# Optimization experiments

Measured on AMD Instinct MI355X. Metric: run time of the kernel, lower is better.

The kernel has to match this reference:

```python
import jax, jax.numpy as jnp
import numpy as np

NEG_SLOPE = 0.2  # PyG GATConv default negative_slope


def gat_conv(x, src, dst, W, a_src, a_dst, b, concat):
    """One PyG-style GATConv (with self-loops already in src/dst).
    x: [N, F_in], W: [F_in, H*C], a_src/a_dst: [H, C], b: [H*C] or [C].
    """
    N = x.shape[0]
    H, C = a_src.shape
    h = (x @ W).reshape(N, H, C)                      # [N,H,C]
    al_s = jnp.einsum('nhc,hc->nh', h, a_src)         # [N,H]
    al_d = jnp.einsum('nhc,hc->nh', h, a_dst)
    e = al_s[src] + al_d[dst]                         # [E,H]
    e = jnp.where(e >= 0, e, NEG_SLOPE * e)           # leaky_relu
    # softmax over edges grouped by destination node
    emax = jax.ops.segment_max(e, dst, num_segments=N)  # [N,H]
    ex = jnp.exp(e - emax[dst])
    denom = jax.ops.segment_sum(ex, dst, num_segments=N)
    alpha = ex / denom[dst]                           # [E,H]
    msg = h[src] * alpha[:, :, None]                  # [E,H,C]
    out = jax.ops.segment_sum(msg, dst, num_segments=N)  # [N,H,C]
    out = out.reshape(N, H * C) if concat else out.mean(axis=1)
    return out + b


def setup_inputs() -> dict:
    key = jax.random.key(0)
    ks = jax.random.split(key, 10)
    N, E = 100000, 1600000
    F_in, Hc, H, F_out = 128, 64, 2, 64
    x = jax.random.normal(ks[0], (N, F_in), dtype=jnp.float32)
    edge_index = jax.random.randint(ks[1], (2, E), 0, N, dtype=jnp.int64)
    s1 = 1.0 / np.sqrt(F_in)
    W1 = jax.random.uniform(ks[2], (F_in, H * Hc), jnp.float32, -s1, s1)
    a_src1 = jax.random.normal(ks[3], (H, Hc), jnp.float32) * 0.1
    a_dst1 = jax.random.normal(ks[4], (H, Hc), jnp.float32) * 0.1
    b1 = jnp.zeros((H * Hc,), jnp.float32)
    s2 = 1.0 / np.sqrt(H * Hc)
    W2 = jax.random.uniform(ks[5], (H * Hc, H * F_out), jnp.float32, -s2, s2)
    a_src2 = jax.random.normal(ks[6], (H, F_out), jnp.float32) * 0.1
    a_dst2 = jax.random.normal(ks[7], (H, F_out), jnp.float32) * 0.1
    b2 = jnp.zeros((F_out,), jnp.float32)
    return {"x": x, "edge_index": edge_index,
            "W1": W1, "a_src1": a_src1, "a_dst1": a_dst1, "b1": b1,
            "W2": W2, "a_src2": a_src2, "a_dst2": a_dst2, "b2": b2}


def reference(x, edge_index, W1, a_src1, a_dst1, b1, W2, a_src2, a_dst2, b2):
    N = x.shape[0]
    loops = jnp.arange(N, dtype=edge_index.dtype)
    src = jnp.concatenate([edge_index[0], loops])  # PyG GATConv adds self-loops
    dst = jnp.concatenate([edge_index[1], loops])
    h = gat_conv(x, src, dst, W1, a_src1, a_dst1, b1, concat=True)
    h = jax.nn.elu(h)
    out = gat_conv(h, src, dst, W2, a_src2, a_dst2, b2, concat=False)
    return out
```

## Files before the change

### kernel.cpp

```cpp
#include <hip/hip_runtime.h>
#include <hip/hip_fp16.h>

#define NEG_SLOPE 0.2f

typedef _Float16 half4v __attribute__((ext_vector_type(4)));
typedef _Float16 half8v __attribute__((ext_vector_type(8)));
typedef float f32x4 __attribute__((ext_vector_type(4)));

__device__ inline unsigned enc_max(float f) {
    unsigned b = __float_as_uint(f);
    return (b & 0x80000000u) ? ~b : (b | 0x80000000u);
}
__device__ inline float dec_max(unsigned k) {
    return (k & 0x80000000u) ? __uint_as_float(k ^ 0x80000000u)
                             : __uint_as_float(~k);
}

__global__ __launch_bounds__(256) void gemm_al_kernel(
    const float* __restrict__ X, const float* __restrict__ W,
    const float* __restrict__ asrc, const float* __restrict__ adst,
    __half* __restrict__ H16, float* __restrict__ AL,
    unsigned* __restrict__ ubp, int N)
{
    __shared__ alignas(16) char smem[49152];

    const int t = threadIdx.x, lane = t & 63, wave = t >> 6;
    const int r0 = blockIdx.x * 64;

#pragma unroll
    for (int i = 0; i < 8; i++) {
        const int f = t + i * 256;
        const int row = f >> 5, k4 = f & 31;
        const int k8 = k4 >> 1, hf = k4 & 1;
        float4 v = make_float4(0.f, 0.f, 0.f, 0.f);
        if (r0 + row < N) v = ((const float4*)X)[(size_t)(r0 + row) * 32 + k4];
        half4v h = { (_Float16)v.x, (_Float16)v.y, (_Float16)v.z, (_Float16)v.w };
        const int slot = row * 16 + (k8 ^ (row & 7));
        *(half4v*)(smem + slot * 16 + hf * 8) = h;
    }
    {
        const int c = t >> 1, kh = t & 1;
        const float* Wc = W + c;
#pragma unroll
        for (int i8 = 0; i8 < 8; i8++) {
            const int k0 = kh * 64 + i8 * 8;
            half8v h;
#pragma unroll
            for (int j = 0; j < 8; j++) h[j] = (_Float16)Wc[(size_t)(k0 + j) * 128];
            const int slot = c * 16 + ((k0 >> 3) ^ (c & 7));
            *(half8v*)(smem + 16384 + slot * 16) = h;
        }
    }
    __syncthreads();

    const int mrow = wave * 16 + (lane & 15);
    const int kg = lane >> 4;
    half4v a[8];
#pragma unroll
    for (int ks = 0; ks < 8; ks++) {
        const int k0 = ks * 16 + kg * 4;
        const int slot = mrow * 16 + ((k0 >> 3) ^ (mrow & 7));
        a[ks] = *(const half4v*)(smem + slot * 16 + (k0 & 7) * 2);
    }
    f32x4 acc[8];
#pragma unroll
    for (int ct = 0; ct < 8; ct++) acc[ct] = (f32x4){0.f, 0.f, 0.f, 0.f};
#pragma unroll
    for (int ct = 0; ct < 8; ct++) {
        const int c = ct * 16 + (lane & 15);
        const char* sbase = smem + 16384 + c * 256;
        const int csw = c & 7;
#pragma unroll
        for (int ks = 0; ks < 8; ks++) {
            const int k0 = ks * 16 + kg * 4;
            const int slot = (k0 >> 3) ^ csw;
            half4v b = *(const half4v*)(sbase + slot * 16 + (k0 & 7) * 2);
            acc[ct] = __builtin_amdgcn_mfma_f32_16x16x16f16(a[ks], b, acc[ct], 0, 0, 0);
        }
    }

    float psh0[4] = {0,0,0,0}, psh1[4] = {0,0,0,0};
    float pdh0[4] = {0,0,0,0}, pdh1[4] = {0,0,0,0};
#pragma unroll
    for (int ct = 0; ct < 8; ct++) {
        const int c = ct * 16 + (lane & 15);
        const float as = asrc[c], ad = adst[c];
#pragma unroll
        for (int r = 0; r < 4; r++) {
            if (ct < 4) { psh0[r] = fmaf(acc[ct][r], as, psh0[r]);
                          pdh0[r] = fmaf(acc[ct][r], ad, pdh0[r]); }
            else        { psh1[r] = fmaf(acc[ct][r], as, psh1[r]);
                          pdh1[r] = fmaf(acc[ct][r], ad, pdh1[r]); }
        }
    }
#pragma unroll
    for (int off = 1; off <= 8; off <<= 1) {
#pragma unroll
        for (int r = 0; r < 4; r++) {
            psh0[r] += __shfl_xor(psh0[r], off, 64);
            psh1[r] += __shfl_xor(psh1[r], off, 64);
            pdh0[r] += __shfl_xor(pdh0[r], off, 64);
            pdh1[r] += __shfl_xor(pdh1[r], off, 64);
        }
    }
    float rmax0 = -__builtin_inff(), rmax1 = -__builtin_inff();
    if ((lane & 15) == 0) {
#pragma unroll
        for (int r = 0; r < 4; r++) {
            const int gr = r0 + wave * 16 + (lane >> 4) * 4 + r;
            if (gr < N) {
                ((float4*)AL)[gr] = make_float4(psh0[r], psh1[r], pdh0[r], pdh1[r]);
                rmax0 = fmaxf(rmax0, psh0[r]);
                rmax1 = fmaxf(rmax1, psh1[r]);
            }
        }
    }
#pragma unroll
    for (int off = 32; off > 0; off >>= 1) {
        rmax0 = fmaxf(rmax0, __shfl_xor(rmax0, off, 64));
        rmax1 = fmaxf(rmax1, __shfl_xor(rmax1, off, 64));
    }

    __syncthreads();
    float* Dst = (float*)smem;
    float* red = (float*)(smem + 33792);
    if (lane == 0) { red[wave * 2] = rmax0; red[wave * 2 + 1] = rmax1; }
#pragma unroll
    for (int ct = 0; ct < 8; ct++) {
        const int col = ct * 16 + (lane & 15);
        float* drow = Dst + wave * 2112 + ((lane >> 4) * 4) * 132 + col;
#pragma unroll
        for (int r = 0; r < 4; r++) drow[r * 132] = acc[ct][r];
    }
    __syncthreads();
    if (t < 2) {
        float m = fmaxf(fmaxf(red[t], red[2 + t]), fmaxf(red[4 + t], red[6 + t]));
        atomicMax(&ubp[t], enc_max(m));
    }
#pragma unroll
    for (int i = 0; i < 4; i++) {
        const int f = t + i * 256;
        const int row = f >> 4, c16 = f & 15;
        if (r0 + row < N) {
            const float* src = Dst + (row >> 4) * 2112 + (row & 15) * 132 + c16 * 8;
            const float4 v0 = *(const float4*)src;
            const float4 v1 = *(const float4*)(src + 4);
            half8v h = { (_Float16)v0.x, (_Float16)v0.y, (_Float16)v0.z, (_Float16)v0.w,
                         (_Float16)v1.x, (_Float16)v1.y, (_Float16)v1.z, (_Float16)v1.w };
            *(half8v*)((_Float16*)H16 + (size_t)(r0 + row) * 128 + c16 * 8) = h;
        }
    }
}

__global__ void count_kernel(const int* __restrict__ edst, int* __restrict__ cnt,
                             int E, int N)
{
    int i = blockIdx.x * 256 + threadIdx.x;
    if (i < E)            atomicAdd(&cnt[edst[i]], 1);
    else if (i < E + N)   atomicAdd(&cnt[i - E], 1);
}

__global__ void scan_local_kernel(const int* __restrict__ in, int* __restrict__ out,
                                  int* __restrict__ bsum, int n)
{
    __shared__ int sm[1024];
    const int t = threadIdx.x;
    const int i = blockIdx.x * 1024 + t;
    int v = (i < n) ? in[i] : 0;
    sm[t] = v;
    __syncthreads();
    for (int off = 1; off < 1024; off <<= 1) {
        int x = (t >= off) ? sm[t - off] : 0;
        __syncthreads();
        sm[t] += x;
        __syncthreads();
    }
    if (i < n) out[i] = sm[t];
    if (t == 1023) bsum[blockIdx.x] = sm[t];
}

__global__ void scan_excl_single_kernel(int* __restrict__ a, int B)
{
    __shared__ int sm[1024];
    const int t = threadIdx.x;
    int v = (t < B) ? a[t] : 0;
    sm[t] = v;
    __syncthreads();
    for (int off = 1; off < 1024; off <<= 1) {
        int x = (t >= off) ? sm[t - off] : 0;
        __syncthreads();
        sm[t] += x;
        __syncthreads();
    }
    if (t < B) a[t] = sm[t] - v;
}

__global__ void finalize_csr_kernel(const int* __restrict__ incl,
                                    const int* __restrict__ cnt,
                                    const int* __restrict__ bexcl,
                                    int* __restrict__ dstptr, int* __restrict__ cursor,
                                    int N, int Etot)
{
    const int i = blockIdx.x * 1024 + threadIdx.x;
    if (i < N) {
        int v = incl[i] + bexcl[i >> 10] - cnt[i];
        dstptr[i] = v;
        cursor[i] = v;
    }
    if (i == N) dstptr[N] = Etot;
}

__global__ void scatter_kernel(const int* __restrict__ esrc, const int* __restrict__ edst,
                               int* __restrict__ cursor, int* __restrict__ ssrc,
                               int E, int N, int sliceN, int bps)
{
    const int slice = blockIdx.x & 7;
    const int dlo = slice * sliceN;
    const int dhi = min(N, dlo + sliceN);
    const int Etot = E + N;
    for (int i = (blockIdx.x >> 3) * 256 + (int)threadIdx.x; i < Etot; i += bps * 256) {
        int s, d;
        if (i < E) { s = esrc[i]; d = edst[i]; }
        else       { s = d = i - E; }
        if (d >= dlo && d < dhi) {
            int pos = atomicAdd(&cursor[d], 1);
            ssrc[pos] = s;
        }
    }
}

__global__ __launch_bounds__(256) void aggregate_kernel(
    const __half* __restrict__ H16, const float* __restrict__ AL,
    const int* __restrict__ dstptr, const int* __restrict__ ssrc,
    const unsigned* __restrict__ ubenc, const float* __restrict__ bias,
    float* __restrict__ out, int N, int mode)
{
    const int wid  = (blockIdx.x * blockDim.x + threadIdx.x) >> 6;
    const int lane = threadIdx.x & 63;
    if (wid * 2 >= N) return;
    const int nl   = lane & 31;
    const int n    = wid * 2 + (lane >> 5);
    const bool act = (n < N);
    const int nn   = act ? n : (N - 1);
    const int beg  = dstptr[nn];
    const int end  = act ? dstptr[nn + 1] : beg;

    const int head = nl >> 4;
    const float ald = AL[(size_t)nn * 4 + 2 + head];
    float ub = dec_max(ubenc[head]) + ald;
    ub = (ub >= 0.f) ? ub : NEG_SLOPE * ub;

    const int nblk = (end - beg + 3) >> 2;
    const int trips = max(nblk, __shfl_xor(nblk, 32, 64));

    float s = 0.f, a0 = 0.f, a1 = 0.f, a2 = 0.f, a3 = 0.f;

    int sA[4];
    float e0[4], e1[4];
    uint2 g0[4], g1[4];

    auto LSRC = [&](int b, int (&sv)[4]) {
#pragma unroll
        for (int k = 0; k < 4; k++) {
            const int idx = beg + 4 * b + k;
            const int v = ssrc[idx];
            sv[k] = (idx < end) ? v : -1;
        }
    };
    auto LHE = [&](const int (&sv)[4], float (&e)[4], uint2 (&g)[4]) {
#pragma unroll
        for (int k = 0; k < 4; k++) {
            const int src = (sv[k] >= 0) ? sv[k] : 0;
            const float a = AL[(size_t)src * 4 + head];
            e[k] = (sv[k] >= 0) ? a : -__builtin_inff();
            g[k] = ((const uint2*)(H16 + (size_t)src * 128))[nl];
        }
    };

    {
        int ta[4], tb[4];
        LSRC(0, ta); LSRC(1, tb); LSRC(2, sA);
        LHE(ta, e0, g0);
        LHE(tb, e1, g1);
    }

    for (int t = 0; t < trips; t++) {
        int sB[4];
        LSRC(t + 3, sB);
        float e2[4]; uint2 g2[4];
        LHE(sA, e2, g2);
#pragma unroll
        for (int k = 0; k < 4; k++) {
            float tt = e0[k] + ald;
            tt = (tt >= 0.f) ? tt : NEG_SLOPE * tt;
            const float p = __expf(tt - ub);
            s += p;
            const __half2* ph = (const __half2*)&g0[k];
            const float2 f01 = __half22float2(ph[0]);
            const float2 f23 = __half22float2(ph[1]);
            a0 = fmaf(p, f01.x, a0);
            a1 = fmaf(p, f01.y, a1);
            a2 = fmaf(p, f23.x, a2);
            a3 = fmaf(p, f23.y, a3);
        }
#pragma unroll
        for (int k = 0; k < 4; k++) {
            e0[k] = e1[k]; g0[k] = g1[k];
            e1[k] = e2[k]; g1[k] = g2[k];
            sA[k] = sB[k];
        }
    }

    if (!act) return;
    const float inv = 1.f / s;
    float o0 = a0 * inv, o1 = a1 * inv, o2 = a2 * inv, o3 = a3 * inv;

    if (mode == 0) {
        const float4 b4 = ((const float4*)bias)[nl];
        o0 += b4.x; o1 += b4.y; o2 += b4.z; o3 += b4.w;
        o0 = (o0 > 0.f) ? o0 : (__expf(o0) - 1.f);
        o1 = (o1 > 0.f) ? o1 : (__expf(o1) - 1.f);
        o2 = (o2 > 0.f) ? o2 : (__expf(o2) - 1.f);
        o3 = (o3 > 0.f) ? o3 : (__expf(o3) - 1.f);
        ((float4*)out)[(size_t)n * 32 + nl] = make_float4(o0, o1, o2, o3);
    } else {
        const float q0 = __shfl_xor(o0, 16, 64);
        const float q1 = __shfl_xor(o1, 16, 64);
        const float q2 = __shfl_xor(o2, 16, 64);
        const float q3 = __shfl_xor(o3, 16, 64);
        if (nl < 16) {
            const float4 b4 = ((const float4*)bias)[nl];
            ((float4*)out)[(size_t)n * 16 + nl] =
                make_float4(0.5f * (o0 + q0) + b4.x, 0.5f * (o1 + q1) + b4.y,
                            0.5f * (o2 + q2) + b4.z, 0.5f * (o3 + q3) + b4.w);
        }
    }
}

extern "C" void kernel_launch(void* const* d_in, const int* in_sizes, int n_in,
                              void* d_out, int out_size, void* d_ws, size_t ws_size,
                              hipStream_t stream)
{
    const float* x   = (const float*)d_in[0];
    const int*   eix = (const int*)d_in[1];
    const float* W1  = (const float*)d_in[2];
    const float* as1 = (const float*)d_in[3];
    const float* ad1 = (const float*)d_in[4];
    const float* b1  = (const float*)d_in[5];
    const float* W2  = (const float*)d_in[6];
    const float* as2 = (const float*)d_in[7];
    const float* ad2 = (const float*)d_in[8];
    const float* b2  = (const float*)d_in[9];
    float* out = (float*)d_out;

    const int N = in_sizes[0] / 128;
    const int E = in_sizes[1] / 2;
    const int Etot = E + N;
    const int* esrc = eix;
    const int* edst = eix + E;

    char* p = (char*)d_ws;
    __half*   h16    = (__half*)p;   p += (size_t)N * 128 * 2;
    float*    y1     = (float*)p;    p += (size_t)N * 128 * 4;
    float*    al     = (float*)p;    p += (size_t)N * 4 * 4;
    int*      cnt    = (int*)p;      p += (size_t)N * 4;
    unsigned* ub     = (unsigned*)p; p += 64;
    int*      incl   = (int*)p;      p += (size_t)N * 4;
    int*      dstptr = (int*)p;      p += (size_t)(N + 1) * 4;
    int*      cursor = (int*)p;      p += (size_t)N * 4;
    int*      bs1    = (int*)p;      p += 1024 * 4;
    int*      ssrc   = (int*)p;      p += (size_t)(Etot + 256) * 4;

    hipMemsetAsync(cnt, 0, (size_t)N * 4 + 64, stream);

    {
        const int eblocks = (Etot + 255) / 256;
        const int B0 = (N + 1023) / 1024;
        count_kernel<<<eblocks, 256, 0, stream>>>(edst, cnt, E, N);
        scan_local_kernel<<<B0, 1024, 0, stream>>>(cnt, incl, bs1, N);
        scan_excl_single_kernel<<<1, 1024, 0, stream>>>(bs1, B0);
        finalize_csr_kernel<<<(N + 1024) / 1024, 1024, 0, stream>>>(
            incl, cnt, bs1, dstptr, cursor, N, Etot);
        const int sliceN = (N + 7) / 8;
        const int bps = 512;
        scatter_kernel<<<bps * 8, 256, 0, stream>>>(esrc, edst, cursor, ssrc,
                                                    E, N, sliceN, bps);
    }

    const int ggrid = (N + 63) / 64;
    const int nwaves = (N + 1) / 2;
    const int ablocks = (nwaves + 3) / 4;

    gemm_al_kernel<<<ggrid, 256, 0, stream>>>(x, W1, as1, ad1, h16, al, ub, N);
    aggregate_kernel<<<ablocks, 256, 0, stream>>>(h16, al, dstptr, ssrc, ub, b1, y1, N, 0);

    gemm_al_kernel<<<ggrid, 256, 0, stream>>>(y1, W2, as2, ad2, h16, al, ub + 2, N);
    aggregate_kernel<<<ablocks, 256, 0, stream>>>(h16, al, dstptr, ssrc, ub + 2, b2, out, N, 1);
}
```

Measured before the change: 377.0 us.

## Map one wavefront per destination node in GAT aggregation with exp2 softmax

The aggregation kernel now gives each destination node a full 64-lane wavefront, with each lane holding two fp16 features, instead of packing two nodes per wave at four features per lane. Each node now loops over its own edge count instead of the larger count of the paired node. The gather pipeline rotates through three register buffers rather than copying them. Per-edge index masking is replaced by a zero-padded tail in the source array plus a zero weight for out-of-range edges. Attention coefficients are pre-scaled by log2(e) in the GEMM so the softmax can use exp2f. The trade-off is twice as many waves with narrower 4-byte gathers per lane, which may increase instruction and scheduling overhead.

```diff
diff --git a/kernel.cpp b/kernel.cpp
--- a/kernel.cpp
+++ b/kernel.cpp
@@ -2,6 +2,7 @@
 #include <hip/hip_fp16.h>
 
 #define NEG_SLOPE 0.2f
+#define LOG2E 1.4426950408889634f
 
 typedef _Float16 half4v __attribute__((ext_vector_type(4)));
 typedef _Float16 half8v __attribute__((ext_vector_type(8)));
@@ -84,7 +85,7 @@
 #pragma unroll
     for (int ct = 0; ct < 8; ct++) {
         const int c = ct * 16 + (lane & 15);
-        const float as = asrc[c], ad = adst[c];
+        const float as = asrc[c] * LOG2E, ad = adst[c] * LOG2E;
 #pragma unroll
         for (int r = 0; r < 4; r++) {
             if (ct < 4) { psh0[r] = fmaf(acc[ct][r], as, psh0[r]);
@@ -229,110 +230,82 @@
     }
 }
 
-__global__ __launch_bounds__(256) void aggregate_kernel(
+__global__ __launch_bounds__(128) void aggregate_kernel(
     const __half* __restrict__ H16, const float* __restrict__ AL,
     const int* __restrict__ dstptr, const int* __restrict__ ssrc,
     const unsigned* __restrict__ ubenc, const float* __restrict__ bias,
     float* __restrict__ out, int N, int mode)
 {
-    const int wid  = (blockIdx.x * blockDim.x + threadIdx.x) >> 6;
+    const int n = (blockIdx.x * blockDim.x + threadIdx.x) >> 6;
     const int lane = threadIdx.x & 63;
-    if (wid * 2 >= N) return;
-    const int nl   = lane & 31;
-    const int n    = wid * 2 + (lane >> 5);
-    const bool act = (n < N);
-    const int nn   = act ? n : (N - 1);
-    const int beg  = dstptr[nn];
-    const int end  = act ? dstptr[nn + 1] : beg;
-
-    const int head = nl >> 4;
-    const float ald = AL[(size_t)nn * 4 + 2 + head];
+    if (n >= N) return;
+
+    const int beg = dstptr[n], end = dstptr[n + 1];
+    const int head = lane >> 5;
+    const float ald = AL[(size_t)n * 4 + 2 + head];
     float ub = dec_max(ubenc[head]) + ald;
-    ub = (ub >= 0.f) ? ub : NEG_SLOPE * ub;
+    ub = fmaxf(ub, NEG_SLOPE * ub);
 
     const int nblk = (end - beg + 3) >> 2;
-    const int trips = max(nblk, __shfl_xor(nblk, 32, 64));
-
-    float s = 0.f, a0 = 0.f, a1 = 0.f, a2 = 0.f, a3 = 0.f;
-
-    int sA[4];
-    float e0[4], e1[4];
-    uint2 g0[4], g1[4];
+
+    float s = 0.f, a0 = 0.f, a1 = 0.f;
+
+    int   sv0[4], sv1[4], sv2[4];
+    float e0[4], e1[4], e2[4];
+    unsigned g0[4], g1[4], g2[4];
 
     auto LSRC = [&](int b, int (&sv)[4]) {
 #pragma unroll
+        for (int k = 0; k < 4; k++) sv[k] = ssrc[beg + 4 * b + k];
+    };
+    auto LHE = [&](const int (&sv)[4], float (&e)[4], unsigned (&g)[4]) {
+#pragma unroll
         for (int k = 0; k < 4; k++) {
-            const int idx = beg + 4 * b + k;
-            const int v = ssrc[idx];
-            sv[k] = (idx < end) ? v : -1;
+            e[k] = AL[(size_t)sv[k] * 4 + head];
+            g[k] = ((const unsigned*)(H16 + (size_t)sv[k] * 128))[lane];
         }
     };
-    auto LHE = [&](const int (&sv)[4], float (&e)[4], uint2 (&g)[4]) {
+    auto COMP = [&](int t, const float (&e)[4], const unsigned (&g)[4]) {
+        const int rem = end - (beg + 4 * t);
 #pragma unroll
         for (int k = 0; k < 4; k++) {
-            const int src = (sv[k] >= 0) ? sv[k] : 0;
-            const float a = AL[(size_t)src * 4 + head];
-            e[k] = (sv[k] >= 0) ? a : -__builtin_inff();
-            g[k] = ((const uint2*)(H16 + (size_t)src * 128))[nl];
+            float tt = e[k] + ald;
+            tt = fmaxf(tt, NEG_SLOPE * tt);
+            float p = exp2f(tt - ub);
+            p = (k < rem) ? p : 0.f;
+            s += p;
+            const float2 f = __half22float2(*(const __half2*)&g[k]);
+            a0 = fmaf(p, f.x, a0);
+            a1 = fmaf(p, f.y, a1);
         }
     };
 
-    {
-        int ta[4], tb[4];
-        LSRC(0, ta); LSRC(1, tb); LSRC(2, sA);
-        LHE(ta, e0, g0);
-        LHE(tb, e1, g1);
-    }
-
-    for (int t = 0; t < trips; t++) {
-        int sB[4];
-        LSRC(t + 3, sB);
-        float e2[4]; uint2 g2[4];
-        LHE(sA, e2, g2);
-#pragma unroll
-        for (int k = 0; k < 4; k++) {
-            float tt = e0[k] + ald;
-            tt = (tt >= 0.f) ? tt : NEG_SLOPE * tt;
-            const float p = __expf(tt - ub);
-            s += p;
-            const __half2* ph = (const __half2*)&g0[k];
-            const float2 f01 = __half22float2(ph[0]);
-            const float2 f23 = __half22float2(ph[1]);
-            a0 = fmaf(p, f01.x, a0);
-            a1 = fmaf(p, f01.y, a1);
-            a2 = fmaf(p, f23.x, a2);
-            a3 = fmaf(p, f23.y, a3);
-        }
-#pragma unroll
-        for (int k = 0; k < 4; k++) {
-            e0[k] = e1[k]; g0[k] = g1[k];
-            e1[k] = e2[k]; g1[k] = g2[k];
-            sA[k] = sB[k];
-        }
-    }
-
-    if (!act) return;
+    LSRC(0, sv0); LSRC(1, sv1); LSRC(2, sv2);
+    LHE(sv0, e0, g0);
+    LHE(sv1, e1, g1);
+
+    for (int t = 0; t < nblk; ) {
+        LHE(sv2, e2, g2); LSRC(t + 3, sv0); COMP(t, e0, g0); if (++t == nblk) break;
+        LHE(sv0, e0, g0); LSRC(t + 3, sv1); COMP(t, e1, g1); if (++t == nblk) break;
+        LHE(sv1, e1, g1); LSRC(t + 3, sv2); COMP(t, e2, g2); if (++t == nblk) break;
+    }
+
     const float inv = 1.f / s;
-    float o0 = a0 * inv, o1 = a1 * inv, o2 = a2 * inv, o3 = a3 * inv;
+    float o0 = a0 * inv, o1 = a1 * inv;
 
     if (mode == 0) {
-        const float4 b4 = ((const float4*)bias)[nl];
-        o0 += b4.x; o1 += b4.y; o2 += b4.z; o3 += b4.w;
+        const float2 b2 = ((const float2*)bias)[lane];
+        o0 += b2.x; o1 += b2.y;
         o0 = (o0 > 0.f) ? o0 : (__expf(o0) - 1.f);
         o1 = (o1 > 0.f) ? o1 : (__expf(o1) - 1.f);
-        o2 = (o2 > 0.f) ? o2 : (__expf(o2) - 1.f);
-        o3 = (o3 > 0.f) ? o3 : (__expf(o3) - 1.f);
-        ((float4*)out)[(size_t)n * 32 + nl] = make_float4(o0, o1, o2, o3);
+        ((float2*)out)[(size_t)n * 64 + lane] = make_float2(o0, o1);
     } else {
-        const float q0 = __shfl_xor(o0, 16, 64);
-        const float q1 = __shfl_xor(o1, 16, 64);
-        const float q2 = __shfl_xor(o2, 16, 64);
-        const float q3 = __shfl_xor(o3, 16, 64);
-        if (nl < 16) {
-            const float4 b4 = ((const float4*)bias)[nl];
-            ((float4*)out)[(size_t)n * 16 + nl] =
-                make_float4(0.5f * (o0 + q0) + b4.x, 0.5f * (o1 + q1) + b4.y,
-                            0.5f * (o2 + q2) + b4.z, 0.5f * (o3 + q3) + b4.w);
+        const float q0 = __shfl_xor(o0, 32, 64);
+        const float q1 = __shfl_xor(o1, 32, 64);
+        if (lane < 32) {
+            const float2 b2 = ((const float2*)bias)[lane];
+            ((float2*)out)[(size_t)n * 32 + lane] =
+                make_float2(0.5f * (o0 + q0) + b2.x, 0.5f * (o1 + q1) + b2.y);
         }
     }
 }
@@ -372,6 +345,7 @@
     int*      ssrc   = (int*)p;      p += (size_t)(Etot + 256) * 4;
 
     hipMemsetAsync(cnt, 0, (size_t)N * 4 + 64, stream);
+    hipMemsetAsync(ssrc + Etot, 0, 256 * 4, stream);
 
     {
         const int eblocks = (Etot + 255) / 256;
@@ -388,12 +362,11 @@
     }
 
     const int ggrid = (N + 63) / 64;
-    const int nwaves = (N + 1) / 2;
-    const int ablocks = (nwaves + 3) / 4;
+    const int ablocks = (N + 1) / 2;
 
     gemm_al_kernel<<<ggrid, 256, 0, stream>>>(x, W1, as1, ad1, h16, al, ub, N);
-    aggregate_kernel<<<ablocks, 256, 0, stream>>>(h16, al, dstptr, ssrc, ub, b1, y1, N, 0);
+    aggregate_kernel<<<ablocks, 128, 0, stream>>>(h16, al, dstptr, ssrc, ub, b1, y1, N, 0);
 
     gemm_al_kernel<<<ggrid, 256, 0, stream>>>(y1, W2, as2, ad2, h16, al, ub + 2, N);
-    aggregate_kernel<<<ablocks, 256, 0, stream>>>(h16, al, dstptr, ssrc, ub + 2, b2, out, N, 1);
-}
+    aggregate_kernel<<<ablocks, 128, 0, stream>>>(h16, al, dstptr, ssrc, ub + 2, b2, out, N, 1);
+}
```

Result: slower. 404.7 us (+7.3%).

## Sort destination nodes by degree for balanced aggregation and simplify gather loop

Applied to the files above, without the earlier changes.

Builds a counting-sort permutation of destination nodes by in-degree during CSR construction, so each wave's two half-wave nodes have similar edge counts and do less divergent idle work. The aggregate loop drops per-edge validity masks on loads by zero-padding the tail of ssrc, and masks only the computed weight. It also rotates three register buffers instead of copying them, and folds log2(e) into the attention coefficients so exp2f replaces __expf. The cost is extra histogram and atomic work in the scan and finalize kernels, plus an indirect order lookup that scatters output writes.

```diff
diff --git a/kernel.cpp b/kernel.cpp
--- a/kernel.cpp
+++ b/kernel.cpp
@@ -2,6 +2,7 @@
 #include <hip/hip_fp16.h>
 
 #define NEG_SLOPE 0.2f
+#define LOG2E 1.4426950408889634f
 
 typedef _Float16 half4v __attribute__((ext_vector_type(4)));
 typedef _Float16 half8v __attribute__((ext_vector_type(8)));
@@ -84,7 +85,7 @@
 #pragma unroll
     for (int ct = 0; ct < 8; ct++) {
         const int c = ct * 16 + (lane & 15);
-        const float as = asrc[c], ad = adst[c];
+        const float as = asrc[c] * LOG2E, ad = adst[c] * LOG2E;
 #pragma unroll
         for (int r = 0; r < 4; r++) {
             if (ct < 4) { psh0[r] = fmaf(acc[ct][r], as, psh0[r]);
@@ -161,14 +162,17 @@
 }
 
 __global__ void scan_local_kernel(const int* __restrict__ in, int* __restrict__ out,
-                                  int* __restrict__ bsum, int n)
+                                  int* __restrict__ bsum, int* __restrict__ hist, int n)
 {
     __shared__ int sm[1024];
+    __shared__ int lh[256];
     const int t = threadIdx.x;
     const int i = blockIdx.x * 1024 + t;
+    if (t < 256) lh[t] = 0;
     int v = (i < n) ? in[i] : 0;
     sm[t] = v;
     __syncthreads();
+    if (i < n) atomicAdd(&lh[min(v, 255)], 1);
     for (int off = 1; off < 1024; off <<= 1) {
         int x = (t >= off) ? sm[t - off] : 0;
         __syncthreads();
@@ -177,9 +181,11 @@
     }
     if (i < n) out[i] = sm[t];
     if (t == 1023) bsum[blockIdx.x] = sm[t];
-}
-
-__global__ void scan_excl_single_kernel(int* __restrict__ a, int B)
+    if (t < 256 && lh[t]) atomicAdd(&hist[t], lh[t]);
+}
+
+__global__ void scan_excl_single_kernel(int* __restrict__ a, int B,
+                                        int* __restrict__ hist)
 {
     __shared__ int sm[1024];
     const int t = threadIdx.x;
@@ -193,21 +199,48 @@
         __syncthreads();
     }
     if (t < B) a[t] = sm[t] - v;
+    __syncthreads();
+    int h = (t < 256) ? hist[t] : 0;
+    sm[t] = h;
+    __syncthreads();
+    for (int off = 1; off < 256; off <<= 1) {
+        int x = (t >= off && t < 256) ? sm[t - off] : 0;
+        __syncthreads();
+        if (t < 256) sm[t] += x;
+        __syncthreads();
+    }
+    if (t < 256) hist[t] = sm[t] - h;
 }
 
 __global__ void finalize_csr_kernel(const int* __restrict__ incl,
                                     const int* __restrict__ cnt,
                                     const int* __restrict__ bexcl,
                                     int* __restrict__ dstptr, int* __restrict__ cursor,
+                                    int* __restrict__ hist, int* __restrict__ order,
                                     int N, int Etot)
 {
-    const int i = blockIdx.x * 1024 + threadIdx.x;
+    __shared__ int lh[256], lbase[256];
+    const int t = threadIdx.x;
+    const int i = blockIdx.x * 1024 + t;
+    if (t < 256) lh[t] = 0;
+    __syncthreads();
+    int bin = 0;
     if (i < N) {
-        int v = incl[i] + bexcl[i >> 10] - cnt[i];
+        const int c = cnt[i];
+        const int v = incl[i] + bexcl[i >> 10] - c;
         dstptr[i] = v;
         cursor[i] = v;
+        bin = min(c, 255);
+        atomicAdd(&lh[bin], 1);
     }
     if (i == N) dstptr[N] = Etot;
+    __syncthreads();
+    if (t < 256) { lbase[t] = lh[t] ? atomicAdd(&hist[t], lh[t]) : 0; lh[t] = 0; }
+    __syncthreads();
+    if (i < N) {
+        const int off = atomicAdd(&lh[bin], 1);
+        order[lbase[bin] + off] = i;
+    }
 }
 
 __global__ void scatter_kernel(const int* __restrict__ esrc, const int* __restrict__ edst,
@@ -232,70 +265,55 @@
 __global__ __launch_bounds__(256) void aggregate_kernel(
     const __half* __restrict__ H16, const float* __restrict__ AL,
     const int* __restrict__ dstptr, const int* __restrict__ ssrc,
-    const unsigned* __restrict__ ubenc, const float* __restrict__ bias,
-    float* __restrict__ out, int N, int mode)
+    const int* __restrict__ order, const unsigned* __restrict__ ubenc,
+    const float* __restrict__ bias, float* __restrict__ out, int N, int mode)
 {
     const int wid  = (blockIdx.x * blockDim.x + threadIdx.x) >> 6;
     const int lane = threadIdx.x & 63;
     if (wid * 2 >= N) return;
+    const int nidx = wid * 2 + (lane >> 5);
+    const bool act = (nidx < N);
+    const int n    = order[act ? nidx : N - 1];
+    const int beg  = dstptr[n];
+    const int edges = act ? (dstptr[n + 1] - beg) : 0;
     const int nl   = lane & 31;
-    const int n    = wid * 2 + (lane >> 5);
-    const bool act = (n < N);
-    const int nn   = act ? n : (N - 1);
-    const int beg  = dstptr[nn];
-    const int end  = act ? dstptr[nn + 1] : beg;
-
     const int head = nl >> 4;
-    const float ald = AL[(size_t)nn * 4 + 2 + head];
+
+    const float ald = AL[(size_t)n * 4 + 2 + head];
     float ub = dec_max(ubenc[head]) + ald;
-    ub = (ub >= 0.f) ? ub : NEG_SLOPE * ub;
-
-    const int nblk = (end - beg + 3) >> 2;
-    const int trips = max(nblk, __shfl_xor(nblk, 32, 64));
+    ub = fmaxf(ub, NEG_SLOPE * ub);
+
+    int tr = (edges + 3) >> 2;
+    tr = max(tr, __shfl_xor(tr, 32, 64));
+    const int trips = tr;
 
     float s = 0.f, a0 = 0.f, a1 = 0.f, a2 = 0.f, a3 = 0.f;
 
-    int sA[4];
-    float e0[4], e1[4];
-    uint2 g0[4], g1[4];
+    int   sv0[4], sv1[4], sv2[4];
+    float e0[4], e1[4], e2[4];
+    uint2 g0[4], g1[4], g2[4];
 
     auto LSRC = [&](int b, int (&sv)[4]) {
 #pragma unroll
-        for (int k = 0; k < 4; k++) {
-            const int idx = beg + 4 * b + k;
-            const int v = ssrc[idx];
-            sv[k] = (idx < end) ? v : -1;
-        }
+        for (int k = 0; k < 4; k++) sv[k] = ssrc[beg + 4 * b + k];
     };
     auto LHE = [&](const int (&sv)[4], float (&e)[4], uint2 (&g)[4]) {
 #pragma unroll
         for (int k = 0; k < 4; k++) {
-            const int src = (sv[k] >= 0) ? sv[k] : 0;
-            const float a = AL[(size_t)src * 4 + head];
-            e[k] = (sv[k] >= 0) ? a : -__builtin_inff();
-            g[k] = ((const uint2*)(H16 + (size_t)src * 128))[nl];
+            e[k] = AL[(size_t)sv[k] * 4 + head];
+            g[k] = ((const uint2*)(H16 + (size_t)sv[k] * 128))[nl];
         }
     };
-
-    {
-        int ta[4], tb[4];
-        LSRC(0, ta); LSRC(1, tb); LSRC(2, sA);
-        LHE(ta, e0, g0);
-        LHE(tb, e1, g1);
-    }
-
-    for (int t = 0; t < trips; t++) {
-        int sB[4];
-        LSRC(t + 3, sB);
-        float e2[4]; uint2 g2[4];
-        LHE(sA, e2, g2);
+    auto COMP = [&](int t, const float (&e)[4], const uint2 (&g)[4]) {
+        const int rem = edges - 4 * t;
 #pragma unroll
         for (int k = 0; k < 4; k++) {
-            float tt = e0[k] + ald;
-            tt = (tt >= 0.f) ? tt : NEG_SLOPE * tt;
-            const float p = __expf(tt - ub);
+            float tt = e[k] + ald;
+            tt = fmaxf(tt, NEG_SLOPE * tt);
+            float p = exp2f(tt - ub);
+            p = (k < rem) ? p : 0.f;
             s += p;
-            const __half2* ph = (const __half2*)&g0[k];
+            const __half2* ph = (const __half2*)&g[k];
             const float2 f01 = __half22float2(ph[0]);
             const float2 f23 = __half22float2(ph[1]);
             a0 = fmaf(p, f01.x, a0);
@@ -303,12 +321,16 @@
             a2 = fmaf(p, f23.x, a2);
             a3 = fmaf(p, f23.y, a3);
         }
-#pragma unroll
-        for (int k = 0; k < 4; k++) {
-            e0[k] = e1[k]; g0[k] = g1[k];
-            e1[k] = e2[k]; g1[k] = g2[k];
-            sA[k] = sB[k];
-        }
+    };
+
+    LSRC(0, sv0); LSRC(1, sv1); LSRC(2, sv2);
+    LHE(sv0, e0, g0);
+    LHE(sv1, e1, g1);
+
+    for (int t = 0; t < trips; ) {
+        LHE(sv2, e2, g2); LSRC(t + 3, sv0); COMP(t, e0, g0); if (++t == trips) break;
+        LHE(sv0, e0, g0); LSRC(t + 3, sv1); COMP(t, e1, g1); if (++t == trips) break;
+        LHE(sv1, e1, g1); LSRC(t + 3, sv2); COMP(t, e2, g2); if (++t == trips) break;
     }
 
     if (!act) return;
@@ -365,22 +387,25 @@
     float*    al     = (float*)p;    p += (size_t)N * 4 * 4;
     int*      cnt    = (int*)p;      p += (size_t)N * 4;
     unsigned* ub     = (unsigned*)p; p += 64;
+    int*      hist   = (int*)p;      p += 256 * 4;
     int*      incl   = (int*)p;      p += (size_t)N * 4;
     int*      dstptr = (int*)p;      p += (size_t)(N + 1) * 4;
     int*      cursor = (int*)p;      p += (size_t)N * 4;
+    int*      order  = (int*)p;      p += (size_t)N * 4;
     int*      bs1    = (int*)p;      p += 1024 * 4;
     int*      ssrc   = (int*)p;      p += (size_t)(Etot + 256) * 4;
 
-    hipMemsetAsync(cnt, 0, (size_t)N * 4 + 64, stream);
+    hipMemsetAsync(cnt, 0, (size_t)N * 4 + 64 + 1024, stream);
+    hipMemsetAsync(ssrc + Etot, 0, 256 * 4, stream);
 
     {
         const int eblocks = (Etot + 255) / 256;
         const int B0 = (N + 1023) / 1024;
         count_kernel<<<eblocks, 256, 0, stream>>>(edst, cnt, E, N);
-        scan_local_kernel<<<B0, 1024, 0, stream>>>(cnt, incl, bs1, N);
-        scan_excl_single_kernel<<<1, 1024, 0, stream>>>(bs1, B0);
+        scan_local_kernel<<<B0, 1024, 0, stream>>>(cnt, incl, bs1, hist, N);
+        scan_excl_single_kernel<<<1, 1024, 0, stream>>>(bs1, B0, hist);
         finalize_csr_kernel<<<(N + 1024) / 1024, 1024, 0, stream>>>(
-            incl, cnt, bs1, dstptr, cursor, N, Etot);
+            incl, cnt, bs1, dstptr, cursor, hist, order, N, Etot);
         const int sliceN = (N + 7) / 8;
         const int bps = 512;
         scatter_kernel<<<bps * 8, 256, 0, stream>>>(esrc, edst, cursor, ssrc,
@@ -388,12 +413,13 @@
     }
 
     const int ggrid = (N + 63) / 64;
-    const int nwaves = (N + 1) / 2;
-    const int ablocks = (nwaves + 3) / 4;
+    const int ablocks = (N + 7) / 8;
 
     gemm_al_kernel<<<ggrid, 256, 0, stream>>>(x, W1, as1, ad1, h16, al, ub, N);
-    aggregate_kernel<<<ablocks, 256, 0, stream>>>(h16, al, dstptr, ssrc, ub, b1, y1, N, 0);
+    aggregate_kernel<<<ablocks, 256, 0, stream>>>(h16, al, dstptr, ssrc, order,
+                                                  ub, b1, y1, N, 0);
 
     gemm_al_kernel<<<ggrid, 256, 0, stream>>>(y1, W2, as2, ad2, h16, al, ub + 2, N);
-    aggregate_kernel<<<ablocks, 256, 0, stream>>>(h16, al, dstptr, ssrc, ub + 2, b2, out, N, 1);
-}
+    aggregate_kernel<<<ablocks, 256, 0, stream>>>(h16, al, dstptr, ssrc, order,
+                                                  ub + 2, b2, out, N, 1);
+}
```

New measurement: 401.2 us. 6.4% more time.

## Slice count kernel by destination, use exp2 logits, rotate aggregate prefetch buffers

Applied to the files above, without the earlier changes.

The count kernel now partitions destination nodes into 8 slices and grid-strides over the edges, matching the scatter kernel, so atomics from each block stay within one slice of the count array. The attention coefficients are pre-scaled by log2(e) so the aggregation can use exp2f. Because leaky ReLU commutes with positive scaling, the softmax is unchanged. The aggregate loop swaps its shift-register prefetch for a three-way rotating buffer, masks padded edges with a lane predicate instead of -inf sentinels, and zeroes the ssrc padding so out-of-range loads read node 0. This is meant to remove register copies and select instructions, at the cost of larger unrolled code and an extra memset.

```diff
diff --git a/kernel.cpp b/kernel.cpp
--- a/kernel.cpp
+++ b/kernel.cpp
@@ -2,6 +2,7 @@
 #include <hip/hip_fp16.h>
 
 #define NEG_SLOPE 0.2f
+#define LOG2E 1.4426950408889634f
 
 typedef _Float16 half4v __attribute__((ext_vector_type(4)));
 typedef _Float16 half8v __attribute__((ext_vector_type(8)));
@@ -84,7 +85,7 @@
 #pragma unroll
     for (int ct = 0; ct < 8; ct++) {
         const int c = ct * 16 + (lane & 15);
-        const float as = asrc[c], ad = adst[c];
+        const float as = asrc[c] * LOG2E, ad = adst[c] * LOG2E;
 #pragma unroll
         for (int r = 0; r < 4; r++) {
             if (ct < 4) { psh0[r] = fmaf(acc[ct][r], as, psh0[r]);
@@ -153,11 +154,16 @@
 }
 
 __global__ void count_kernel(const int* __restrict__ edst, int* __restrict__ cnt,
-                             int E, int N)
-{
-    int i = blockIdx.x * 256 + threadIdx.x;
-    if (i < E)            atomicAdd(&cnt[edst[i]], 1);
-    else if (i < E + N)   atomicAdd(&cnt[i - E], 1);
+                             int E, int N, int sliceN, int bps)
+{
+    const int slice = blockIdx.x & 7;
+    const int dlo = slice * sliceN;
+    const int dhi = min(N, dlo + sliceN);
+    const int Etot = E + N;
+    for (int i = (blockIdx.x >> 3) * 256 + (int)threadIdx.x; i < Etot; i += bps * 256) {
+        const int d = (i < E) ? edst[i] : (i - E);
+        if (d >= dlo && d < dhi) atomicAdd(&cnt[d], 1);
+    }
 }
 
 __global__ void scan_local_kernel(const int* __restrict__ in, int* __restrict__ out,
@@ -238,64 +244,53 @@
     const int wid  = (blockIdx.x * blockDim.x + threadIdx.x) >> 6;
     const int lane = threadIdx.x & 63;
     if (wid * 2 >= N) return;
-    const int nl   = lane & 31;
     const int n    = wid * 2 + (lane >> 5);
     const bool act = (n < N);
     const int nn   = act ? n : (N - 1);
     const int beg  = dstptr[nn];
-    const int end  = act ? dstptr[nn + 1] : beg;
-
+    const int edges = act ? (dstptr[nn + 1] - beg) : 0;
+    const int nl   = lane & 31;
     const int head = nl >> 4;
+
     const float ald = AL[(size_t)nn * 4 + 2 + head];
     float ub = dec_max(ubenc[head]) + ald;
-    ub = (ub >= 0.f) ? ub : NEG_SLOPE * ub;
-
-    const int nblk = (end - beg + 3) >> 2;
-    const int trips = max(nblk, __shfl_xor(nblk, 32, 64));
+    ub = fmaxf(ub, NEG_SLOPE * ub);
+
+    int tr = (edges + 3) >> 2;
+    tr = max(tr, __shfl_xor(tr, 32, 64));
+    const int trips = tr;
 
     float s = 0.f, a0 = 0.f, a1 = 0.f, a2 = 0.f, a3 = 0.f;
 
-    int sA[4];
-    float e0[4], e1[4];
-    uint2 g0[4], g1[4];
+    int   sv0[4], sv1[4], sv2[4];
+    float e0[4], e1[4], e2[4];
+    uint2 g0[4], g1[4], g2[4];
 
     auto LSRC = [&](int b, int (&sv)[4]) {
 #pragma unroll
         for (int k = 0; k < 4; k++) {
-            const int idx = beg + 4 * b + k;
-            const int v = ssrc[idx];
-            sv[k] = (idx < end) ? v : -1;
+            const int idx = 4 * b + k;
+            const int v = ssrc[beg + idx];
+            sv[k] = (idx < edges) ? v : 0;
         }
     };
     auto LHE = [&](const int (&sv)[4], float (&e)[4], uint2 (&g)[4]) {
 #pragma unroll
         for (int k = 0; k < 4; k++) {
-            const int src = (sv[k] >= 0) ? sv[k] : 0;
-            const float a = AL[(size_t)src * 4 + head];
-            e[k] = (sv[k] >= 0) ? a : -__builtin_inff();
-            g[k] = ((const uint2*)(H16 + (size_t)src * 128))[nl];
+            e[k] = AL[(size_t)sv[k] * 4 + head];
+            g[k] = ((const uint2*)(H16 + (size_t)sv[k] * 128))[nl];
         }
     };
-
-    {
-        int ta[4], tb[4];
-        LSRC(0, ta); LSRC(1, tb); LSRC(2, sA);
-        LHE(ta, e0, g0);
-        LHE(tb, e1, g1);
-    }
-
-    for (int t = 0; t < trips; t++) {
-        int sB[4];
-        LSRC(t + 3, sB);
-        float e2[4]; uint2 g2[4];
-        LHE(sA, e2, g2);
+    auto COMP = [&](int t, const float (&e)[4], const uint2 (&g)[4]) {
+        const int rem = edges - 4 * t;
 #pragma unroll
         for (int k = 0; k < 4; k++) {
-            float tt = e0[k] + ald;
-            tt = (tt >= 0.f) ? tt : NEG_SLOPE * tt;
-            const float p = __expf(tt - ub);
+            float tt = e[k] + ald;
+            tt = fmaxf(tt, NEG_SLOPE * tt);
+            float p = exp2f(tt - ub);
+            p = (k < rem) ? p : 0.f;
             s += p;
-            const __half2* ph = (const __half2*)&g0[k];
+            const __half2* ph = (const __half2*)&g[k];
             const float2 f01 = __half22float2(ph[0]);
             const float2 f23 = __half22float2(ph[1]);
             a0 = fmaf(p, f01.x, a0);
@@ -303,12 +298,16 @@
             a2 = fmaf(p, f23.x, a2);
             a3 = fmaf(p, f23.y, a3);
         }
-#pragma unroll
-        for (int k = 0; k < 4; k++) {
-            e0[k] = e1[k]; g0[k] = g1[k];
-            e1[k] = e2[k]; g1[k] = g2[k];
-            sA[k] = sB[k];
-        }
+    };
+
+    LSRC(0, sv0); LSRC(1, sv1); LSRC(2, sv2);
+    LHE(sv0, e0, g0);
+    LHE(sv1, e1, g1);
+
+    for (int t = 0; t < trips; ) {
+        LHE(sv2, e2, g2); LSRC(t + 3, sv0); COMP(t, e0, g0); if (++t == trips) break;
+        LHE(sv0, e0, g0); LSRC(t + 3, sv1); COMP(t, e1, g1); if (++t == trips) break;
+        LHE(sv1, e1, g1); LSRC(t + 3, sv2); COMP(t, e2, g2); if (++t == trips) break;
     }
 
     if (!act) return;
@@ -372,24 +371,23 @@
     int*      ssrc   = (int*)p;      p += (size_t)(Etot + 256) * 4;
 
     hipMemsetAsync(cnt, 0, (size_t)N * 4 + 64, stream);
+    hipMemsetAsync(ssrc + Etot, 0, 256 * 4, stream);
 
     {
-        const int eblocks = (Etot + 255) / 256;
         const int B0 = (N + 1023) / 1024;
-        count_kernel<<<eblocks, 256, 0, stream>>>(edst, cnt, E, N);
+        const int sliceN = (N + 7) / 8;
+        const int bps = 512;
+        count_kernel<<<bps * 8, 256, 0, stream>>>(edst, cnt, E, N, sliceN, bps);
         scan_local_kernel<<<B0, 1024, 0, stream>>>(cnt, incl, bs1, N);
         scan_excl_single_kernel<<<1, 1024, 0, stream>>>(bs1, B0);
         finalize_csr_kernel<<<(N + 1024) / 1024, 1024, 0, stream>>>(
             incl, cnt, bs1, dstptr, cursor, N, Etot);
-        const int sliceN = (N + 7) / 8;
-        const int bps = 512;
         scatter_kernel<<<bps * 8, 256, 0, stream>>>(esrc, edst, cursor, ssrc,
                                                     E, N, sliceN, bps);
     }
 
     const int ggrid = (N + 63) / 64;
-    const int nwaves = (N + 1) / 2;
-    const int ablocks = (nwaves + 3) / 4;
+    const int ablocks = (N + 7) / 8;
 
     gemm_al_kernel<<<ggrid, 256, 0, stream>>>(x, W1, as1, ad1, h16, al, ub, N);
     aggregate_kernel<<<ablocks, 256, 0, stream>>>(h16, al, dstptr, ssrc, ub, b1, y1, N, 0);
```

Result: slower. 385.5 us (+2.2%).
